# Performance work log

Measured on AMD Instinct MI355X. Metric: run time of the kernel, lower is better.

Reference implementation:

```python
import jax, jax.numpy as jnp
import numpy as np

EPS = 1e-13

def masked_softmax(scores, mask):
    # scores: (B, L1, L2), mask: (B, L2) float {0,1}
    m = mask[:, None, :]
    # faithful to ESIM masked_softmax: softmax(scores * mask), re-mask, renormalize
    p = jax.nn.softmax(scores * m, axis=-1) * m
    return p / (jnp.sum(p, axis=-1, keepdims=True) + EPS)

def weighted_sum(values, weights, mask):
    # values: (B, Lv, H), weights: (B, Lq, Lv), mask: (B, Lq)
    out = jnp.einsum('bqv,bvh->bqh', weights, values)
    return out * mask[:, :, None]

def setup_inputs() -> dict:
    key = jax.random.key(0)
    k1, k2, k3, k4 = jax.random.split(key, 4)
    B, P, Q, H = 64, 1024, 1024, 256
    pre_batch = jax.random.normal(k1, (B, P, H), dtype=jnp.float32)
    hypo_batch = jax.random.normal(k2, (B, Q, H), dtype=jnp.float32)
    pre_mask = jax.random.randint(k3, (B, P), 0, 2, dtype=jnp.int32).at[:, 0].set(1)
    hypo_mask = jax.random.randint(k4, (B, Q), 0, 2, dtype=jnp.int32).at[:, 0].set(1)
    return {"pre_batch": pre_batch, "pre_mask": pre_mask,
            "hypo_batch": hypo_batch, "hypo_mask": hypo_mask}

def reference(pre_batch, pre_mask, hypo_batch, hypo_mask):
    pre_m = pre_mask.astype(pre_batch.dtype)
    hypo_m = hypo_mask.astype(hypo_batch.dtype)
    # similarity: (B, P, Q)
    similarity = jnp.einsum('bph,bqh->bpq', pre_batch, hypo_batch)
    pre_hypo_attn = masked_softmax(similarity, hypo_m)                       # (B,P,Q)
    hypo_pre_attn = masked_softmax(jnp.swapaxes(similarity, 1, 2), pre_m)    # (B,Q,P)
    attented_pre = weighted_sum(hypo_batch, pre_hypo_attn, pre_m)            # (B,P,H)
    attented_hypo = weighted_sum(pre_batch, hypo_pre_attn, hypo_m)           # (B,Q,H)
    return (attented_pre, attented_hypo)
```

## Files before the change

### kernel.cpp

```cpp
#include <hip/hip_runtime.h>
#include <stdint.h>

#define NB 64
#define NN 1024
#define NH 256

typedef _Float16 h8v __attribute__((ext_vector_type(8)));
typedef float    f4v __attribute__((ext_vector_type(4)));
typedef uint32_t u4v __attribute__((ext_vector_type(4)));
typedef uint32_t u2v __attribute__((ext_vector_type(2)));

static __device__ __forceinline__ uint32_t pack2h(float a, float b) {
  uint32_t ua = (uint32_t)__builtin_bit_cast(uint16_t, (_Float16)a);
  uint32_t ub = (uint32_t)__builtin_bit_cast(uint16_t, (_Float16)b);
  return ua | (ub << 16);
}

static __device__ __forceinline__ void gl_lds16(const void* g, void* l) {
  __builtin_amdgcn_global_load_lds(
      (const __attribute__((address_space(1))) uint32_t*)g,
      (__attribute__((address_space(3))) uint32_t*)l, 16, 0, 0);
}

__global__ __launch_bounds__(256)
void prep_tiles(const float* __restrict__ pre, const float* __restrict__ hypo,
                uint8_t* __restrict__ img)
{
  const int id = blockIdx.x;
  const int m  = id >> 11;
  const int bt = id & 2047;
  const float* src = (m ? hypo : pre) + (size_t)bt * (32 * NH);
  uint8_t* kimg = img + (size_t)id * 32768;
  uint8_t* vimg = kimg + 16384;

  __shared__ __align__(16) float ft[32 * 260];
  const int t = threadIdx.x, w = t >> 6, lane = t & 63;

#pragma unroll
  for (int i = 0; i < 8; ++i) {
    const int row = w * 8 + i;
    gl_lds16(src + row * NH + lane * 4, (uint8_t*)ft + row * 1040);
  }
  __syncthreads();

#pragma unroll
  for (int c = 0; c < 4; ++c) {
    const int k = c * 8 + (t >> 5);
    const uint32_t X = (uint32_t)((t & 31) * 16);
    const uint32_t h0 = ((X >> 4) ^ (uint32_t)(k & 7)) * 8;
    const uint8_t* p = (const uint8_t*)ft + k * 1040 + h0 * 4;
    f4v a0 = *(const f4v*)p;
    f4v a1 = *(const f4v*)(p + 16);
    u4v o; o[0] = pack2h(a0[0], a0[1]); o[1] = pack2h(a0[2], a0[3]);
    o[2] = pack2h(a1[0], a1[1]); o[3] = pack2h(a1[2], a1[3]);
    *(u4v*)(kimg + c * 4096 + t * 16) = o;
  }
#pragma unroll
  for (int c = 0; c < 4; ++c) {
    const int h  = c * 64 + (t >> 2);
    const int k8 = 8 * (t & 3);
    float v[8];
#pragma unroll
    for (int j = 0; j < 8; ++j) v[j] = ft[(k8 + j) * 260 + h];
    u4v o; o[0] = pack2h(v[0], v[1]); o[1] = pack2h(v[2], v[3]);
    o[2] = pack2h(v[4], v[5]); o[3] = pack2h(v[6], v[7]);
    *(u4v*)(vimg + c * 4096 + t * 16) = o;
  }
}

__global__ __launch_bounds__(256, 2)
void attn_img(const uint8_t* __restrict__ img,
              const int* __restrict__ pre_mask, const int* __restrict__ hypo_mask,
              float* __restrict__ out)
{
  const int fid  = blockIdx.x;
  const int xcd  = fid & 7;
  const int s    = fid >> 3;
  const int bp   = xcd * 16 + (s >> 3);
  const int rblk = s & 7;
  const int pass = bp >> 6;
  const int b    = bp & 63;

  const uint8_t* qimg  = img + (size_t)(pass ? 1 : 0) * 67108864;
  const uint8_t* kvimg = img + (size_t)(pass ? 0 : 1) * 67108864;
  const int* kmask = pass == 0 ? hypo_mask : pre_mask;
  const int* qmask = pass == 0 ? pre_mask  : hypo_mask;
  float* outp = out + ((size_t)pass * NB + b) * NN * NH;
  const uint8_t* kvb = kvimg + (size_t)b * (32 * 32768);
  const int* kmb = kmask + b * NN;

  __shared__ __align__(16) uint8_t sbuf[2][32768];

  const int t    = threadIdx.x;
  const int lane = t & 63;
  const int w    = t >> 6;
  const int g    = lane >> 4;
  const int q    = lane & 15;

  h8v qf0[8], qf1[8];
  {
    const uint8_t* qb = qimg + (size_t)b * (32 * 32768);
#pragma unroll
    for (int ff = 0; ff < 2; ++ff) {
      const int qrow = rblk * 128 + w * 32 + ff * 16 + q;
      const uint8_t* qt = qb + (size_t)(qrow >> 5) * 32768 + (qrow & 31) * 512;
      const uint32_t swq = (uint32_t)((qrow & 7) << 4);
#pragma unroll
      for (int c = 0; c < 8; ++c) {
        h8v v = *(const h8v*)(qt + (((uint32_t)((c * 4 + g) << 4)) ^ swq));
        if (ff == 0) qf0[c] = v; else qf1[c] = v;
      }
    }
  }

  f4v accA[16], accB[16];
#pragma unroll
  for (int cf = 0; cf < 16; ++cf) { accA[cf] = (f4v){0,0,0,0}; accB[cf] = (f4v){0,0,0,0}; }
  float mrunA = -1e30f, lrunA = 0.f, mrunB = -1e30f, lrunB = 0.f;

#pragma unroll
  for (int i = 0; i < 8; ++i)
    gl_lds16(kvb + w * 8192 + i * 1024 + lane * 16, &sbuf[0][0] + w * 8192 + i * 1024);
  __syncthreads();

#pragma unroll 1
  for (int kt = 0; kt < 32; ++kt) {
    const int cur = kt & 1;
    if (kt < 31) {
      const uint8_t* kvt = kvb + (size_t)(kt + 1) * 32768;
#pragma unroll
      for (int i = 0; i < 8; ++i)
        gl_lds16(kvt + w * 8192 + i * 1024 + lane * 16,
                 &sbuf[cur ^ 1][0] + w * 8192 + i * 1024);
    }
    const uint8_t* sK = &sbuf[cur][0];
    const uint8_t* sV = sK + 16384;
    const int kb = kt * 32;

    int msk0[4], msk1[4];
#pragma unroll
    for (int r = 0; r < 4; ++r) {
      msk0[r] = kmb[kb + 4 * g + r];
      msk1[r] = kmb[kb + 16 + 4 * g + r];
    }

    f4v s0A = (f4v){0,0,0,0}, s1A = (f4v){0,0,0,0};
    f4v s0B = (f4v){0,0,0,0}, s1B = (f4v){0,0,0,0};
#pragma unroll
    for (int c = 0; c < 8; ++c) {
      const uint32_t a0 = (uint32_t)(q * 512) + (((uint32_t)(c * 64 + g * 16)) ^ ((uint32_t)((q & 7) << 4)));
      h8v k0 = *(const h8v*)(sK + a0);
      h8v k1 = *(const h8v*)(sK + a0 + 8192);
      s0A = __builtin_amdgcn_mfma_f32_16x16x32_f16(k0, qf0[c], s0A, 0, 0, 0);
      s0B = __builtin_amdgcn_mfma_f32_16x16x32_f16(k0, qf1[c], s0B, 0, 0, 0);
      s1A = __builtin_amdgcn_mfma_f32_16x16x32_f16(k1, qf0[c], s1A, 0, 0, 0);
      s1B = __builtin_amdgcn_mfma_f32_16x16x32_f16(k1, qf1[c], s1B, 0, 0, 0);
    }

    h8v apA, apB;
#pragma unroll
    for (int ff = 0; ff < 2; ++ff) {
      f4v s0 = ff ? s0B : s0A, s1 = ff ? s1B : s1A;
      float mrun = ff ? mrunB : mrunA, lrun = ff ? lrunB : lrunA;

      float tmax = -1e30f;
#pragma unroll
      for (int r = 0; r < 4; ++r)
        tmax = fmaxf(tmax, fmaxf(msk0[r] ? s0[r] : -1e30f, msk1[r] ? s1[r] : -1e30f));
      tmax = fmaxf(tmax, __shfl_xor(tmax, 16));
      tmax = fmaxf(tmax, __shfl_xor(tmax, 32));
      const float mnew = fmaxf(mrun, tmax);
      const float scl = __expf(mrun - mnew);

      float p[8];
      float psum = 0.f;
#pragma unroll
      for (int r = 0; r < 4; ++r) {
        float p0 = msk0[r] ? __expf(s0[r] - mnew) : 0.f;
        float p1 = msk1[r] ? __expf(s1[r] - mnew) : 0.f;
        p[r] = p0; p[4 + r] = p1;
        psum += p0 + p1;
      }
      psum += __shfl_xor(psum, 16);
      psum += __shfl_xor(psum, 32);

      if (ff) { lrunB = lrun * scl + psum; mrunB = mnew; }
      else    { lrunA = lrun * scl + psum; mrunA = mnew; }

      float srow[4];
#pragma unroll
      for (int r = 0; r < 4; ++r) srow[r] = __shfl(scl, 4 * g + r);
#pragma unroll
      for (int cf = 0; cf < 16; ++cf) {
#pragma unroll
        for (int r = 0; r < 4; ++r) {
          if (ff) accB[cf][r] *= srow[r]; else accA[cf][r] *= srow[r];
        }
      }

      uint32_t pf00 = pack2h(p[0], p[1]);
      uint32_t pf01 = pack2h(p[2], p[3]);
      uint32_t pf10 = pack2h(p[4], p[5]);
      uint32_t pf11 = pack2h(p[6], p[7]);
      const int srcA = q + 16 * ((2 * g) & 3);
      const int srcB = srcA + 16;
      uint32_t w0a = __shfl(pf00, srcA), w1a = __shfl(pf01, srcA);
      uint32_t w0b = __shfl(pf00, srcB), w1b = __shfl(pf01, srcB);
      uint32_t x0a = __shfl(pf10, srcA), x1a = __shfl(pf11, srcA);
      uint32_t x0b = __shfl(pf10, srcB), x1b = __shfl(pf11, srcB);
      u4v au;
      au[0] = (g >= 2) ? x0a : w0a;
      au[1] = (g >= 2) ? x1a : w1a;
      au[2] = (g >= 2) ? x0b : w0b;
      au[3] = (g >= 2) ? x1b : w1b;
      if (ff) apB = __builtin_bit_cast(h8v, au); else apA = __builtin_bit_cast(h8v, au);
    }

#pragma unroll
    for (int cf = 0; cf < 16; ++cf) {
      h8v bv = *(const h8v*)(sV + (uint32_t)((cf * 16 + q) * 64 + g * 16));
      accA[cf] = __builtin_amdgcn_mfma_f32_16x16x32_f16(apA, bv, accA[cf], 0, 0, 0);
      accB[cf] = __builtin_amdgcn_mfma_f32_16x16x32_f16(apB, bv, accB[cf], 0, 0, 0);
    }

    __syncthreads();
  }

#pragma unroll
  for (int ff = 0; ff < 2; ++ff) {
    const float lrun = ff ? lrunB : lrunA;
    float fac[4];
#pragma unroll
    for (int r = 0; r < 4; ++r) {
      const float lr = __shfl(lrun, 4 * g + r);
      const int row = rblk * 128 + w * 32 + ff * 16 + 4 * g + r;
      fac[r] = (float)qmask[b * NN + row] / lr;
    }
    float* op = outp + (size_t)(rblk * 128 + w * 32 + ff * 16) * NH;
#pragma unroll
    for (int cf = 0; cf < 16; ++cf) {
#pragma unroll
      for (int r = 0; r < 4; ++r) {
        float v = ff ? accB[cf][r] : accA[cf][r];
        op[(4 * g + r) * NH + cf * 16 + q] = v * fac[r];
      }
    }
  }
}

__global__ __launch_bounds__(256, 2)
void fused_dual_attn_fb(const float* __restrict__ pre,  const int* __restrict__ pre_mask,
                        const float* __restrict__ hypo, const int* __restrict__ hypo_mask,
                        float* __restrict__ out)
{
  const int pass = blockIdx.z;
  const float* Qm  = pass == 0 ? pre  : hypo;
  const float* KVm = pass == 0 ? hypo : pre;
  const int* kmask = pass == 0 ? hypo_mask : pre_mask;
  const int* qmask = pass == 0 ? pre_mask  : hypo_mask;
  float* outp = out + (size_t)pass * NB * NN * NH;

  const int b  = blockIdx.y;
  const int r0 = blockIdx.x * 64;

  __shared__ __align__(16) unsigned char sK [32 * NH * 2];
  __shared__ __align__(16) unsigned char sVt[NH * 16 * 4];
  __shared__ int smask[NN];

  const int t    = threadIdx.x;
  const int lane = t & 63;
  const int w    = t >> 6;
  const int g    = lane >> 4;
  const int q    = lane & 15;

  for (int i = t; i < NN; i += 256) smask[i] = kmask[b * NN + i];

  const int qrow = r0 + w * 16 + q;
  h8v qf[8];
  {
    const float* qp = Qm + ((size_t)b * NN + qrow) * NH + g * 8;
#pragma unroll
    for (int c = 0; c < 8; ++c) {
      f4v a0 = *(const f4v*)(qp + c * 32);
      f4v a1 = *(const f4v*)(qp + c * 32 + 4);
      h8v v;
      v[0] = (_Float16)a0[0]; v[1] = (_Float16)a0[1];
      v[2] = (_Float16)a0[2]; v[3] = (_Float16)a0[3];
      v[4] = (_Float16)a1[0]; v[5] = (_Float16)a1[1];
      v[6] = (_Float16)a1[2]; v[7] = (_Float16)a1[3];
      qf[c] = v;
    }
  }

  f4v acc[16];
#pragma unroll
  for (int cf = 0; cf < 16; ++cf) acc[cf] = (f4v){0.f, 0.f, 0.f, 0.f};
  float mrun = -1e30f, lrun = 0.f;

  const int skey = t & 31;
  const int m16  = (t >> 1) & 15;
  const int scb  = (t >> 5) << 2;
  const int odd  = skey & 1;

  for (int kb = 0; kb < NN; kb += 32) {
    __syncthreads();
#pragma unroll
    for (int i = 0; i < 8; ++i) {
      const int col = scb + 32 * i;
      f4v v = *(const f4v*)(KVm + ((size_t)b * NN + kb + skey) * NH + col);
      u2v d; d[0] = pack2h(v[0], v[1]); d[1] = pack2h(v[2], v[3]);
      uint32_t ka = (uint32_t)(skey * 512 + col * 2) ^ (uint32_t)((skey & 7) << 4);
      *(u2v*)(sK + ka) = d;
      float e = odd ? v[0] : v[2];
      float f = odd ? v[1] : v[3];
      float oe = __shfl_xor(e, 1);
      float of = __shfl_xor(f, 1);
      float lo0 = odd ? oe   : v[0];
      float hi0 = odd ? v[2] : oe;
      float lo1 = odd ? of   : v[1];
      float hi1 = odd ? v[3] : of;
      const int h0 = col + odd * 2;
      *(uint32_t*)(sVt + (uint32_t)((h0    ) * 64 + m16 * 4)) = pack2h(lo0, hi0);
      *(uint32_t*)(sVt + (uint32_t)((h0 + 1) * 64 + m16 * 4)) = pack2h(lo1, hi1);
    }
    __syncthreads();

    f4v s0 = (f4v){0.f,0.f,0.f,0.f}, s1 = (f4v){0.f,0.f,0.f,0.f};
#pragma unroll
    for (int c = 0; c < 8; ++c) {
      uint32_t a0 = ((uint32_t)(q * 512 + c * 64 + g * 16)) ^ (uint32_t)((q & 7) << 4);
      uint32_t a1 = ((uint32_t)((16 + q) * 512 + c * 64 + g * 16)) ^ (uint32_t)((q & 7) << 4);
      h8v k0 = *(const h8v*)(sK + a0);
      h8v k1 = *(const h8v*)(sK + a1);
      s0 = __builtin_amdgcn_mfma_f32_16x16x32_f16(k0, qf[c], s0, 0, 0, 0);
      s1 = __builtin_amdgcn_mfma_f32_16x16x32_f16(k1, qf[c], s1, 0, 0, 0);
    }

    int msk[8];
#pragma unroll
    for (int r = 0; r < 4; ++r) {
      msk[r]     = smask[kb + 4 * g + r];
      msk[4 + r] = smask[kb + 16 + 4 * g + r];
    }
    float tmax = -1e30f;
#pragma unroll
    for (int r = 0; r < 4; ++r)
      tmax = fmaxf(tmax, fmaxf(msk[r] ? s0[r] : -1e30f, msk[4 + r] ? s1[r] : -1e30f));
    tmax = fmaxf(tmax, __shfl_xor(tmax, 16));
    tmax = fmaxf(tmax, __shfl_xor(tmax, 32));
    const float mnew = fmaxf(mrun, tmax);
    const float scl = __expf(mrun - mnew);
    mrun = mnew;

    float p[8];
    float psum = 0.f;
#pragma unroll
    for (int r = 0; r < 4; ++r) {
      float p0 = msk[r]     ? __expf(s0[r] - mnew) : 0.f;
      float p1 = msk[4 + r] ? __expf(s1[r] - mnew) : 0.f;
      p[r] = p0; p[4 + r] = p1;
      psum += p0 + p1;
    }
    psum += __shfl_xor(psum, 16);
    psum += __shfl_xor(psum, 32);
    lrun = lrun * scl + psum;

    float srow[4];
#pragma unroll
    for (int r = 0; r < 4; ++r) srow[r] = __shfl(scl, 4 * g + r);
#pragma unroll
    for (int cf = 0; cf < 16; ++cf) {
#pragma unroll
      for (int r = 0; r < 4; ++r) acc[cf][r] *= srow[r];
    }

    uint32_t pf00 = pack2h(p[0], p[1]);
    uint32_t pf01 = pack2h(p[2], p[3]);
    uint32_t pf10 = pack2h(p[4], p[5]);
    uint32_t pf11 = pack2h(p[6], p[7]);
    const int srcA = q + 16 * ((2 * g) & 3);
    const int srcB = srcA + 16;
    uint32_t w0a = __shfl(pf00, srcA), w1a = __shfl(pf01, srcA);
    uint32_t w0b = __shfl(pf00, srcB), w1b = __shfl(pf01, srcB);
    uint32_t x0a = __shfl(pf10, srcA), x1a = __shfl(pf11, srcA);
    uint32_t x0b = __shfl(pf10, srcB), x1b = __shfl(pf11, srcB);
    u4v au;
    au[0] = (g >= 2) ? x0a : w0a;
    au[1] = (g >= 2) ? x1a : w1a;
    au[2] = (g >= 2) ? x0b : w0b;
    au[3] = (g >= 2) ? x1b : w1b;
    const h8v ap = __builtin_bit_cast(h8v, au);

#pragma unroll
    for (int cf = 0; cf < 16; ++cf) {
      h8v bv = *(const h8v*)(sVt + (uint32_t)((cf * 16 + q) * 64 + g * 16));
      acc[cf] = __builtin_amdgcn_mfma_f32_16x16x32_f16(ap, bv, acc[cf], 0, 0, 0);
    }
  }

  float fac[4];
#pragma unroll
  for (int r = 0; r < 4; ++r) {
    const float lr = __shfl(lrun, 4 * g + r);
    const int row = r0 + w * 16 + 4 * g + r;
    fac[r] = (float)qmask[b * NN + row] / lr;
  }
  float* op = outp + ((size_t)b * NN + r0 + w * 16) * NH;
#pragma unroll
  for (int cf = 0; cf < 16; ++cf) {
#pragma unroll
    for (int r = 0; r < 4; ++r) {
      op[(4 * g + r) * NH + cf * 16 + q] = acc[cf][r] * fac[r];
    }
  }
}

extern "C" void kernel_launch(void* const* d_in, const int* in_sizes, int n_in,
                              void* d_out, int out_size, void* d_ws, size_t ws_size,
                              hipStream_t stream) {
  const float* pre       = (const float*)d_in[0];
  const int*   pre_mask  = (const int*)d_in[1];
  const float* hypo      = (const float*)d_in[2];
  const int*   hypo_mask = (const int*)d_in[3];
  float* out = (float*)d_out;
  (void)in_sizes; (void)n_in; (void)out_size;

  if (ws_size >= (size_t)2 * 67108864) {
    uint8_t* img = (uint8_t*)d_ws;
    prep_tiles<<<dim3(4096), dim3(256), 0, stream>>>(pre, hypo, img);
    attn_img<<<dim3(1024), dim3(256), 0, stream>>>(img, pre_mask, hypo_mask, out);
  } else {
    fused_dual_attn_fb<<<dim3(16, 64, 2), dim3(256), 0, stream>>>(pre, pre_mask, hypo, hypo_mask, out);
  }
}
```

Before: 268.7 us.

## Add lazy online-softmax rescaling, interleave A/B softmax, and raise MFMA priority

The online softmax now rescales the running max, sum and the 128 accumulator values only when some row's tile max exceeds the running max by more than 8, decided wave-wide with __any. Otherwise the exponentials are taken against a stale max. This removes most per-tile accumulator multiplies and exp calls, and interleaving the two row-group computations gives more instruction-level parallelism. s_setprio raises wave priority around the MFMA loops so matrix work from different waves can overlap other waves' softmax VALU work. The risk is that fp16 P values can reach up to e^8 relative to the stale max, which reduces precision headroom.

New measurement: 236.4 us. -12.0%, faster.

```diff
diff --git a/kernel.cpp b/kernel.cpp
--- a/kernel.cpp
+++ b/kernel.cpp
@@ -146,6 +146,7 @@
 
     f4v s0A = (f4v){0,0,0,0}, s1A = (f4v){0,0,0,0};
     f4v s0B = (f4v){0,0,0,0}, s1B = (f4v){0,0,0,0};
+    __builtin_amdgcn_s_setprio(1);
 #pragma unroll
     for (int c = 0; c < 8; ++c) {
       const uint32_t a0 = (uint32_t)(q * 512) + (((uint32_t)(c * 64 + g * 16)) ^ ((uint32_t)((q & 7) << 4)));
@@ -156,72 +157,91 @@
       s1A = __builtin_amdgcn_mfma_f32_16x16x32_f16(k1, qf0[c], s1A, 0, 0, 0);
       s1B = __builtin_amdgcn_mfma_f32_16x16x32_f16(k1, qf1[c], s1B, 0, 0, 0);
     }
-
-    h8v apA, apB;
-#pragma unroll
-    for (int ff = 0; ff < 2; ++ff) {
-      f4v s0 = ff ? s0B : s0A, s1 = ff ? s1B : s1A;
-      float mrun = ff ? mrunB : mrunA, lrun = ff ? lrunB : lrunA;
-
-      float tmax = -1e30f;
-#pragma unroll
-      for (int r = 0; r < 4; ++r)
-        tmax = fmaxf(tmax, fmaxf(msk0[r] ? s0[r] : -1e30f, msk1[r] ? s1[r] : -1e30f));
-      tmax = fmaxf(tmax, __shfl_xor(tmax, 16));
-      tmax = fmaxf(tmax, __shfl_xor(tmax, 32));
-      const float mnew = fmaxf(mrun, tmax);
-      const float scl = __expf(mrun - mnew);
-
-      float p[8];
-      float psum = 0.f;
+    __builtin_amdgcn_s_setprio(0);
+
+    float tA = -1e30f, tB = -1e30f;
+#pragma unroll
+    for (int r = 0; r < 4; ++r) {
+      tA = fmaxf(tA, fmaxf(msk0[r] ? s0A[r] : -1e30f, msk1[r] ? s1A[r] : -1e30f));
+      tB = fmaxf(tB, fmaxf(msk0[r] ? s0B[r] : -1e30f, msk1[r] ? s1B[r] : -1e30f));
+    }
+    tA = fmaxf(tA, __shfl_xor(tA, 16));  tB = fmaxf(tB, __shfl_xor(tB, 16));
+    tA = fmaxf(tA, __shfl_xor(tA, 32));  tB = fmaxf(tB, __shfl_xor(tB, 32));
+
+    const bool grow = __any(fmaxf(tA - mrunA, tB - mrunB) > 8.0f);
+    if (grow) {
+      const float mnA = fmaxf(mrunA, tA), mnB = fmaxf(mrunB, tB);
+      const float sA = __expf(mrunA - mnA), sB = __expf(mrunB - mnB);
+      mrunA = mnA; mrunB = mnB;
+      lrunA *= sA; lrunB *= sB;
+      float srA[4], srB[4];
 #pragma unroll
       for (int r = 0; r < 4; ++r) {
-        float p0 = msk0[r] ? __expf(s0[r] - mnew) : 0.f;
-        float p1 = msk1[r] ? __expf(s1[r] - mnew) : 0.f;
-        p[r] = p0; p[4 + r] = p1;
-        psum += p0 + p1;
+        srA[r] = __shfl(sA, 4 * g + r);
+        srB[r] = __shfl(sB, 4 * g + r);
       }
-      psum += __shfl_xor(psum, 16);
-      psum += __shfl_xor(psum, 32);
-
-      if (ff) { lrunB = lrun * scl + psum; mrunB = mnew; }
-      else    { lrunA = lrun * scl + psum; mrunA = mnew; }
-
-      float srow[4];
-#pragma unroll
-      for (int r = 0; r < 4; ++r) srow[r] = __shfl(scl, 4 * g + r);
 #pragma unroll
       for (int cf = 0; cf < 16; ++cf) {
 #pragma unroll
         for (int r = 0; r < 4; ++r) {
-          if (ff) accB[cf][r] *= srow[r]; else accA[cf][r] *= srow[r];
+          accA[cf][r] *= srA[r];
+          accB[cf][r] *= srB[r];
         }
       }
-
-      uint32_t pf00 = pack2h(p[0], p[1]);
-      uint32_t pf01 = pack2h(p[2], p[3]);
-      uint32_t pf10 = pack2h(p[4], p[5]);
-      uint32_t pf11 = pack2h(p[6], p[7]);
+    }
+
+    float pA[8], pB[8];
+    float psA = 0.f, psB = 0.f;
+#pragma unroll
+    for (int r = 0; r < 4; ++r) {
+      float a0 = msk0[r] ? __expf(s0A[r] - mrunA) : 0.f;
+      float a1 = msk1[r] ? __expf(s1A[r] - mrunA) : 0.f;
+      float b0 = msk0[r] ? __expf(s0B[r] - mrunB) : 0.f;
+      float b1 = msk1[r] ? __expf(s1B[r] - mrunB) : 0.f;
+      pA[r] = a0; pA[4 + r] = a1; psA += a0 + a1;
+      pB[r] = b0; pB[4 + r] = b1; psB += b0 + b1;
+    }
+    psA += __shfl_xor(psA, 16);  psB += __shfl_xor(psB, 16);
+    psA += __shfl_xor(psA, 32);  psB += __shfl_xor(psB, 32);
+    lrunA += psA; lrunB += psB;
+
+    h8v apA, apB;
+    {
       const int srcA = q + 16 * ((2 * g) & 3);
       const int srcB = srcA + 16;
-      uint32_t w0a = __shfl(pf00, srcA), w1a = __shfl(pf01, srcA);
-      uint32_t w0b = __shfl(pf00, srcB), w1b = __shfl(pf01, srcB);
-      uint32_t x0a = __shfl(pf10, srcA), x1a = __shfl(pf11, srcA);
-      uint32_t x0b = __shfl(pf10, srcB), x1b = __shfl(pf11, srcB);
-      u4v au;
-      au[0] = (g >= 2) ? x0a : w0a;
-      au[1] = (g >= 2) ? x1a : w1a;
-      au[2] = (g >= 2) ? x0b : w0b;
-      au[3] = (g >= 2) ? x1b : w1b;
-      if (ff) apB = __builtin_bit_cast(h8v, au); else apA = __builtin_bit_cast(h8v, au);
-    }
-
+      uint32_t Af00 = pack2h(pA[0], pA[1]), Af01 = pack2h(pA[2], pA[3]);
+      uint32_t Af10 = pack2h(pA[4], pA[5]), Af11 = pack2h(pA[6], pA[7]);
+      uint32_t Bf00 = pack2h(pB[0], pB[1]), Bf01 = pack2h(pB[2], pB[3]);
+      uint32_t Bf10 = pack2h(pB[4], pB[5]), Bf11 = pack2h(pB[6], pB[7]);
+      uint32_t Aw0a = __shfl(Af00, srcA), Aw1a = __shfl(Af01, srcA);
+      uint32_t Aw0b = __shfl(Af00, srcB), Aw1b = __shfl(Af01, srcB);
+      uint32_t Ax0a = __shfl(Af10, srcA), Ax1a = __shfl(Af11, srcA);
+      uint32_t Ax0b = __shfl(Af10, srcB), Ax1b = __shfl(Af11, srcB);
+      uint32_t Bw0a = __shfl(Bf00, srcA), Bw1a = __shfl(Bf01, srcA);
+      uint32_t Bw0b = __shfl(Bf00, srcB), Bw1b = __shfl(Bf01, srcB);
+      uint32_t Bx0a = __shfl(Bf10, srcA), Bx1a = __shfl(Bf11, srcA);
+      uint32_t Bx0b = __shfl(Bf10, srcB), Bx1b = __shfl(Bf11, srcB);
+      u4v au, bu;
+      au[0] = (g >= 2) ? Ax0a : Aw0a;
+      au[1] = (g >= 2) ? Ax1a : Aw1a;
+      au[2] = (g >= 2) ? Ax0b : Aw0b;
+      au[3] = (g >= 2) ? Ax1b : Aw1b;
+      bu[0] = (g >= 2) ? Bx0a : Bw0a;
+      bu[1] = (g >= 2) ? Bx1a : Bw1a;
+      bu[2] = (g >= 2) ? Bx0b : Bw0b;
+      bu[3] = (g >= 2) ? Bx1b : Bw1b;
+      apA = __builtin_bit_cast(h8v, au);
+      apB = __builtin_bit_cast(h8v, bu);
+    }
+
+    __builtin_amdgcn_s_setprio(1);
 #pragma unroll
     for (int cf = 0; cf < 16; ++cf) {
       h8v bv = *(const h8v*)(sV + (uint32_t)((cf * 16 + q) * 64 + g * 16));
       accA[cf] = __builtin_amdgcn_mfma_f32_16x16x32_f16(apA, bv, accA[cf], 0, 0, 0);
       accB[cf] = __builtin_amdgcn_mfma_f32_16x16x32_f16(apB, bv, accB[cf], 0, 0, 0);
     }
+    __builtin_amdgcn_s_setprio(0);
 
     __syncthreads();
   }
```
